# Kernel optimization log

Measured on AMD Instinct MI355X. Metric: run time of the kernel, lower is better.

The kernel has to match this reference:

```python
import jax, jax.numpy as jnp
import numpy as np

B, Q, N, K, C = 32, 500, 200, 16, 92
CLASS_COST, POLY_COST, GIOU_COST = 1.0, 5.0, 1.0
EPS = 1e-6


def setup_inputs() -> dict:
    key = jax.random.key(0)
    k1, k2, k3, k4 = jax.random.split(key, 4)
    return {
        "pred_logits": jax.random.normal(k1, (B, Q, C), dtype=jnp.float32),
        "pred_polylines": jax.random.uniform(k2, (B, Q, K, 2), dtype=jnp.float32),
        "tgt_labels": jax.random.randint(k3, (B, N), 0, 91, dtype=jnp.int32),
        "tgt_polylines": jax.random.uniform(k4, (B, N, K, 2), dtype=jnp.float32),
    }


def _poly_to_bbox(p):
    # p: (..., K, 2) -> (..., 4) xyxy
    x, y = p[..., 0], p[..., 1]
    return jnp.stack([x.min(-1), y.min(-1), x.max(-1), y.max(-1)], axis=-1)


def _giou(b1, b2):
    # b1: (B,Q,4), b2: (B,N,4) -> (B,Q,N) pairwise generalized IoU
    area1 = jnp.clip(b1[..., 2] - b1[..., 0], 0) * jnp.clip(b1[..., 3] - b1[..., 1], 0)
    area2 = jnp.clip(b2[..., 2] - b2[..., 0], 0) * jnp.clip(b2[..., 3] - b2[..., 1], 0)
    lt = jnp.maximum(b1[:, :, None, :2], b2[:, None, :, :2])
    rb = jnp.minimum(b1[:, :, None, 2:], b2[:, None, :, 2:])
    wh = jnp.clip(rb - lt, 0)
    inter = wh[..., 0] * wh[..., 1]
    union = area1[:, :, None] + area2[:, None, :] - inter
    iou = inter / jnp.maximum(union, EPS)
    lt_c = jnp.minimum(b1[:, :, None, :2], b2[:, None, :, :2])
    rb_c = jnp.maximum(b1[:, :, None, 2:], b2[:, None, :, 2:])
    wh_c = jnp.clip(rb_c - lt_c, 0)
    area_c = wh_c[..., 0] * wh_c[..., 1]
    return iou - (area_c - union) / jnp.maximum(area_c, EPS)


def reference(pred_logits, pred_polylines, tgt_labels, tgt_polylines):
    # Batched matching cost matrix C: (B, Q, N). The host-side scipy Hungarian
    # solve in the original consumes this matrix; the GPU math being kerneled
    # is exactly this cost computation.
    b, q, k = pred_polylines.shape[0], pred_polylines.shape[1], pred_polylines.shape[2]
    n = tgt_labels.shape[1]
    two_k = 2 * k

    prob = jax.nn.softmax(pred_logits, axis=-1)  # (B,Q,C)
    idx = jnp.broadcast_to(tgt_labels[:, None, :], (b, q, n))
    cost_class = -jnp.take_along_axis(prob, idx, axis=2)  # (B,Q,N)

    out_flat = pred_polylines.reshape(b, q, two_k)
    tgt_flat = tgt_polylines.reshape(b, n, two_k)
    tgt_rev = jnp.flip(tgt_polylines, axis=2).reshape(b, n, two_k)
    # L1 cdist, normalized by 2K; take min over polyline orientation
    cost_fwd = jnp.abs(out_flat[:, :, None, :] - tgt_flat[:, None, :, :]).sum(-1) / float(two_k)
    cost_rev = jnp.abs(out_flat[:, :, None, :] - tgt_rev[:, None, :, :]).sum(-1) / float(two_k)
    cost_poly = jnp.minimum(cost_fwd, cost_rev)

    out_bbox = _poly_to_bbox(pred_polylines)  # (B,Q,4)
    tgt_bbox = _poly_to_bbox(tgt_polylines)   # (B,N,4)
    cost_giou = -_giou(out_bbox, tgt_bbox)    # (B,Q,N)

    return CLASS_COST * cost_class + POLY_COST * cost_poly + GIOU_COST * cost_giou
```

## Files before the change

### kernel.cpp

```cpp
#include <hip/hip_runtime.h>
#include <math.h>

constexpr int B_ = 32, Q_ = 500, N_ = 200, K_ = 16, C_ = 92;
constexpr int TWO_K = 2 * K_;
constexpr int WAVES = 8;
constexpr int THREADS = 64 * WAVES;
constexpr int TPAD = 34;
constexpr float EPS_ = 1e-6f;
constexpr float POLY_SCALE = 5.0f / 32.0f;

__device__ __forceinline__ float rfl(float v) {
    return __int_as_float(__builtin_amdgcn_readfirstlane(__float_as_int(v)));
}

__global__ __launch_bounds__(THREADS, 8)
void matcher_cost_kernel(const float* __restrict__ logits,
                         const float* __restrict__ ppoly,
                         const int*   __restrict__ labels,
                         const float* __restrict__ tpoly,
                         float* __restrict__ out)
{
    __shared__ float sT[N_ * TPAD];
    __shared__ float sTB[N_ * 5];
    __shared__ int   sLbl[N_];
    __shared__ float sProb[WAVES * C_];

    const int tid  = threadIdx.x;
    const int b    = blockIdx.y;
    const int q0   = blockIdx.x * WAVES;
    const int w    = tid >> 6;
    const int lane = tid & 63;
    const int q    = q0 + w;

    {
        const float* tb_base = tpoly + (size_t)b * (N_ * TWO_K);
        for (int u = tid; u < N_ * TWO_K / 4; u += THREADS) {
            float4 v = reinterpret_cast<const float4*>(tb_base)[u];
            int n = u >> 3;
            int j = (u & 7) * 4;
            float* d = &sT[n * TPAD + j];
            reinterpret_cast<float2*>(d)[0] = make_float2(v.x, v.y);
            reinterpret_cast<float2*>(d)[1] = make_float2(v.z, v.w);
        }
        for (int n = tid; n < N_; n += THREADS) sLbl[n] = labels[b * N_ + n];
    }
    __syncthreads();

    for (int n = tid; n < N_; n += THREADS) {
        const float2* tr = reinterpret_cast<const float2*>(&sT[n * TPAD]);
        float xm = INFINITY, ym = INFINITY, xM = -INFINITY, yM = -INFINITY;
        #pragma unroll
        for (int k = 0; k < K_; ++k) {
            float2 t = tr[k];
            xm = fminf(xm, t.x); xM = fmaxf(xM, t.x);
            ym = fminf(ym, t.y); yM = fmaxf(yM, t.y);
        }
        sTB[n * 5 + 0] = xm; sTB[n * 5 + 1] = ym;
        sTB[n * 5 + 2] = xM; sTB[n * 5 + 3] = yM;
        sTB[n * 5 + 4] = (xM - xm) * (yM - ym);
    }
    __syncthreads();

    if (q >= Q_) return;

    const int wq = __builtin_amdgcn_readfirstlane(q);
    const float* pp = ppoly + ((size_t)(b * Q_ + wq)) * TWO_K;
    float pfs[TWO_K];
    #pragma unroll
    for (int j = 0; j < TWO_K; ++j) pfs[j] = rfl(pp[j]);

    float pxm, pym, pxM, pyM;
    {
        float2 p = reinterpret_cast<const float2*>(pp)[lane & 15];
        float xm = p.x, xM = p.x, ym = p.y, yM = p.y;
        #pragma unroll
        for (int off = 8; off; off >>= 1) {
            xm = fminf(xm, __shfl_xor(xm, off));
            xM = fmaxf(xM, __shfl_xor(xM, off));
            ym = fminf(ym, __shfl_xor(ym, off));
            yM = fmaxf(yM, __shfl_xor(yM, off));
        }
        pxm = rfl(xm); pxM = rfl(xM); pym = rfl(ym); pyM = rfl(yM);
    }
    const float parea = (pxM - pxm) * (pyM - pym);

    {
        const float* lg = logits + ((size_t)(b * Q_ + wq)) * C_;
        float lv0 = lg[lane];
        float lv1 = (lane < C_ - 64) ? lg[64 + lane] : -INFINITY;
        float m = fmaxf(lv0, lv1);
        #pragma unroll
        for (int off = 32; off; off >>= 1) m = fmaxf(m, __shfl_xor(m, off));
        float e0 = __expf(lv0 - m);
        float e1 = (lane < C_ - 64) ? __expf(lv1 - m) : 0.0f;
        float s = e0 + e1;
        #pragma unroll
        for (int off = 32; off; off >>= 1) s += __shfl_xor(s, off);
        float rs = 1.0f / s;
        sProb[w * C_ + lane] = e0 * rs;
        if (lane < C_ - 64) sProb[w * C_ + 64 + lane] = e1 * rs;
    }

    float* outRow = out + ((size_t)(b * Q_ + wq)) * N_;
    const float* probRow = &sProb[w * C_];

    for (int i = 0; i < (N_ + 63) / 64; ++i) {
        int n = lane + 64 * i;
        if (n >= N_) break;
        const float2* tr = reinterpret_cast<const float2*>(&sT[n * TPAD]);
        float f0 = 0.0f, f1 = 0.0f, r0 = 0.0f, r1 = 0.0f;
        #pragma unroll
        for (int k = 0; k < K_; ++k) {
            float2 t = tr[k];
            float a = fabsf(pfs[2 * k]     - t.x) + fabsf(pfs[2 * k + 1] - t.y);
            float c = fabsf(pfs[30 - 2 * k] - t.x) + fabsf(pfs[31 - 2 * k] - t.y);
            if (k & 1) { f1 += a; r1 += c; } else { f0 += a; r0 += c; }
        }
        float cpoly = fminf(f0 + f1, r0 + r1) * POLY_SCALE;

        float cclass = -probRow[sLbl[n]];

        float tx0 = sTB[n * 5 + 0], ty0 = sTB[n * 5 + 1];
        float tx1 = sTB[n * 5 + 2], ty1 = sTB[n * 5 + 3];
        float tarea = sTB[n * 5 + 4];
        float ix0 = fmaxf(pxm, tx0), iy0 = fmaxf(pym, ty0);
        float ix1 = fminf(pxM, tx1), iy1 = fminf(pyM, ty1);
        float iw = fmaxf(ix1 - ix0, 0.0f), ih = fmaxf(iy1 - iy0, 0.0f);
        float inter = iw * ih;
        float uni = parea + tarea - inter;
        float iou = inter / fmaxf(uni, EPS_);
        float cx0 = fminf(pxm, tx0), cy0 = fminf(pym, ty0);
        float cx1 = fmaxf(pxM, tx1), cy1 = fmaxf(pyM, ty1);
        float ca = (cx1 - cx0) * (cy1 - cy0);
        float giou = iou - (ca - uni) / fmaxf(ca, EPS_);

        outRow[n] = cclass + cpoly - giou;
    }
}

extern "C" void kernel_launch(void* const* d_in, const int* in_sizes, int n_in,
                              void* d_out, int out_size, void* d_ws, size_t ws_size,
                              hipStream_t stream) {
    const float* logits = (const float*)d_in[0];
    const float* ppoly  = (const float*)d_in[1];
    const int*   labels = (const int*)d_in[2];
    const float* tpoly  = (const float*)d_in[3];
    float* out = (float*)d_out;

    dim3 grid((Q_ + WAVES - 1) / WAVES, B_);
    matcher_cost_kernel<<<grid, THREADS, 0, stream>>>(logits, ppoly, labels, tpoly, out);
}
```

Measured before the change: 29.27 us.

## Retile matcher kernel into query-by-target blocks with lanes over queries

```diff
diff --git a/kernel.cpp b/kernel.cpp
--- a/kernel.cpp
+++ b/kernel.cpp
@@ -3,126 +3,129 @@
 
 constexpr int B_ = 32, Q_ = 500, N_ = 200, K_ = 16, C_ = 92;
 constexpr int TWO_K = 2 * K_;
+constexpr int QT = 64;
+constexpr int NG = 50;
 constexpr int WAVES = 8;
 constexpr int THREADS = 64 * WAVES;
-constexpr int TPAD = 34;
+constexpr int PS = 93;
+constexpr int OS = 51;
 constexpr float EPS_ = 1e-6f;
 constexpr float POLY_SCALE = 5.0f / 32.0f;
 
-__device__ __forceinline__ float rfl(float v) {
-    return __int_as_float(__builtin_amdgcn_readfirstlane(__float_as_int(v)));
-}
-
-__global__ __launch_bounds__(THREADS, 8)
+__global__ __launch_bounds__(THREADS)
 void matcher_cost_kernel(const float* __restrict__ logits,
                          const float* __restrict__ ppoly,
                          const int*   __restrict__ labels,
                          const float* __restrict__ tpoly,
                          float* __restrict__ out)
 {
-    __shared__ float sT[N_ * TPAD];
-    __shared__ float sTB[N_ * 5];
-    __shared__ int   sLbl[N_];
-    __shared__ float sProb[WAVES * C_];
+    __shared__ float sProb[QT * PS];
+    __shared__ float sOut[QT * OS];
+    __shared__ float sTB[NG * 5];
 
     const int tid  = threadIdx.x;
-    const int b    = blockIdx.y;
-    const int q0   = blockIdx.x * WAVES;
     const int w    = tid >> 6;
     const int lane = tid & 63;
-    const int q    = q0 + w;
+    const int qt   = blockIdx.x;
+    const int ng   = blockIdx.y;
+    const int b    = blockIdx.z;
+    const int q0   = qt * QT;
+    const int n0   = ng * NG;
 
     {
-        const float* tb_base = tpoly + (size_t)b * (N_ * TWO_K);
-        for (int u = tid; u < N_ * TWO_K / 4; u += THREADS) {
-            float4 v = reinterpret_cast<const float4*>(tb_base)[u];
-            int n = u >> 3;
-            int j = (u & 7) * 4;
-            float* d = &sT[n * TPAD + j];
-            reinterpret_cast<float2*>(d)[0] = make_float2(v.x, v.y);
-            reinterpret_cast<float2*>(d)[1] = make_float2(v.z, v.w);
+        int g = tid >> 3, sub = tid & 7;
+        int qq = q0 + g; if (qq >= Q_) qq = Q_ - 1;
+        const float* lg = logits + ((size_t)(b * Q_ + qq)) * C_;
+        float v[12]; float mx = -INFINITY;
+        #pragma unroll
+        for (int m = 0; m < 12; ++m) {
+            int c = sub + 8 * m;
+            if (c < C_) { v[m] = lg[c]; mx = fmaxf(mx, v[m]); } else v[m] = -INFINITY;
         }
-        for (int n = tid; n < N_; n += THREADS) sLbl[n] = labels[b * N_ + n];
+        #pragma unroll
+        for (int off = 4; off; off >>= 1) mx = fmaxf(mx, __shfl_xor(mx, off, 8));
+        float s = 0.0f;
+        #pragma unroll
+        for (int m = 0; m < 12; ++m) {
+            int c = sub + 8 * m;
+            if (c < C_) { v[m] = __expf(v[m] - mx); s += v[m]; }
+        }
+        #pragma unroll
+        for (int off = 4; off; off >>= 1) s += __shfl_xor(s, off, 8);
+        float rs = 1.0f / s;
+        #pragma unroll
+        for (int m = 0; m < 12; ++m) {
+            int c = sub + 8 * m;
+            if (c < C_) sProb[g * PS + c] = v[m] * rs;
+        }
     }
+
+    {
+        int g = tid >> 3, sub = tid & 7;
+        if (g < NG) {
+            const float4* tr = reinterpret_cast<const float4*>(
+                tpoly + ((size_t)(b * N_ + n0 + g)) * TWO_K);
+            float4 p = tr[sub];
+            float xm = fminf(p.x, p.z), xM = fmaxf(p.x, p.z);
+            float ym = fminf(p.y, p.w), yM = fmaxf(p.y, p.w);
+            #pragma unroll
+            for (int off = 4; off; off >>= 1) {
+                xm = fminf(xm, __shfl_xor(xm, off, 8));
+                xM = fmaxf(xM, __shfl_xor(xM, off, 8));
+                ym = fminf(ym, __shfl_xor(ym, off, 8));
+                yM = fmaxf(yM, __shfl_xor(yM, off, 8));
+            }
+            if (sub == 0) {
+                sTB[g * 5 + 0] = xm; sTB[g * 5 + 1] = ym;
+                sTB[g * 5 + 2] = xM; sTB[g * 5 + 3] = yM;
+                sTB[g * 5 + 4] = (xM - xm) * (yM - ym);
+            }
+        }
+    }
+
+    int qc = q0 + lane; if (qc >= Q_) qc = Q_ - 1;
+    float px[K_], py[K_];
+    float pxm = INFINITY, pxM = -INFINITY, pym = INFINITY, pyM = -INFINITY;
+    {
+        const float4* pr = reinterpret_cast<const float4*>(
+            ppoly + ((size_t)(b * Q_ + qc)) * TWO_K);
+        #pragma unroll
+        for (int j = 0; j < 8; ++j) {
+            float4 v = pr[j];
+            px[2 * j] = v.x;  py[2 * j] = v.y;
+            px[2 * j + 1] = v.z; py[2 * j + 1] = v.w;
+            pxm = fminf(pxm, fminf(v.x, v.z)); pxM = fmaxf(pxM, fmaxf(v.x, v.z));
+            pym = fminf(pym, fminf(v.y, v.w)); pyM = fmaxf(pyM, fmaxf(v.y, v.w));
+        }
+    }
+    const float parea = (pxM - pxm) * (pyM - pym);
     __syncthreads();
 
-    for (int n = tid; n < N_; n += THREADS) {
-        const float2* tr = reinterpret_cast<const float2*>(&sT[n * TPAD]);
-        float xm = INFINITY, ym = INFINITY, xM = -INFINITY, yM = -INFINITY;
+    const int probbase = lane * PS;
+
+    for (int nn = w; nn < NG; nn += WAVES) {
+        const int nu = __builtin_amdgcn_readfirstlane(n0 + nn);
+        const float* __restrict__ tr = tpoly + ((size_t)(b * N_ + nu)) * TWO_K;
+        float ts[TWO_K];
+        #pragma unroll
+        for (int j = 0; j < TWO_K; ++j) ts[j] = tr[j];
+        const int lbl = labels[b * N_ + nu];
+
+        float f0 = 0, f1 = 0, r0 = 0, r1 = 0;
         #pragma unroll
         for (int k = 0; k < K_; ++k) {
-            float2 t = tr[k];
-            xm = fminf(xm, t.x); xM = fmaxf(xM, t.x);
-            ym = fminf(ym, t.y); yM = fmaxf(yM, t.y);
+            float tx = ts[2 * k], ty = ts[2 * k + 1];
+            float af = fabsf(px[k] - tx) + fabsf(py[k] - ty);
+            float ar = fabsf(px[K_ - 1 - k] - tx) + fabsf(py[K_ - 1 - k] - ty);
+            if (k & 1) { f1 += af; r1 += ar; } else { f0 += af; r0 += ar; }
         }
-        sTB[n * 5 + 0] = xm; sTB[n * 5 + 1] = ym;
-        sTB[n * 5 + 2] = xM; sTB[n * 5 + 3] = yM;
-        sTB[n * 5 + 4] = (xM - xm) * (yM - ym);
-    }
-    __syncthreads();
+        float cpoly = fminf(f0 + f1, r0 + r1);
 
-    if (q >= Q_) return;
+        float cclass = -sProb[probbase + lbl];
 
-    const int wq = __builtin_amdgcn_readfirstlane(q);
-    const float* pp = ppoly + ((size_t)(b * Q_ + wq)) * TWO_K;
-    float pfs[TWO_K];
-    #pragma unroll
-    for (int j = 0; j < TWO_K; ++j) pfs[j] = rfl(pp[j]);
-
-    float pxm, pym, pxM, pyM;
-    {
-        float2 p = reinterpret_cast<const float2*>(pp)[lane & 15];
-        float xm = p.x, xM = p.x, ym = p.y, yM = p.y;
-        #pragma unroll
-        for (int off = 8; off; off >>= 1) {
-            xm = fminf(xm, __shfl_xor(xm, off));
-            xM = fmaxf(xM, __shfl_xor(xM, off));
-            ym = fminf(ym, __shfl_xor(ym, off));
-            yM = fmaxf(yM, __shfl_xor(yM, off));
-        }
-        pxm = rfl(xm); pxM = rfl(xM); pym = rfl(ym); pyM = rfl(yM);
-    }
-    const float parea = (pxM - pxm) * (pyM - pym);
-
-    {
-        const float* lg = logits + ((size_t)(b * Q_ + wq)) * C_;
-        float lv0 = lg[lane];
-        float lv1 = (lane < C_ - 64) ? lg[64 + lane] : -INFINITY;
-        float m = fmaxf(lv0, lv1);
-        #pragma unroll
-        for (int off = 32; off; off >>= 1) m = fmaxf(m, __shfl_xor(m, off));
-        float e0 = __expf(lv0 - m);
-        float e1 = (lane < C_ - 64) ? __expf(lv1 - m) : 0.0f;
-        float s = e0 + e1;
-        #pragma unroll
-        for (int off = 32; off; off >>= 1) s += __shfl_xor(s, off);
-        float rs = 1.0f / s;
-        sProb[w * C_ + lane] = e0 * rs;
-        if (lane < C_ - 64) sProb[w * C_ + 64 + lane] = e1 * rs;
-    }
-
-    float* outRow = out + ((size_t)(b * Q_ + wq)) * N_;
-    const float* probRow = &sProb[w * C_];
-
-    for (int i = 0; i < (N_ + 63) / 64; ++i) {
-        int n = lane + 64 * i;
-        if (n >= N_) break;
-        const float2* tr = reinterpret_cast<const float2*>(&sT[n * TPAD]);
-        float f0 = 0.0f, f1 = 0.0f, r0 = 0.0f, r1 = 0.0f;
-        #pragma unroll
-        for (int k = 0; k < K_; ++k) {
-            float2 t = tr[k];
-            float a = fabsf(pfs[2 * k]     - t.x) + fabsf(pfs[2 * k + 1] - t.y);
-            float c = fabsf(pfs[30 - 2 * k] - t.x) + fabsf(pfs[31 - 2 * k] - t.y);
-            if (k & 1) { f1 += a; r1 += c; } else { f0 += a; r0 += c; }
-        }
-        float cpoly = fminf(f0 + f1, r0 + r1) * POLY_SCALE;
-
-        float cclass = -probRow[sLbl[n]];
-
-        float tx0 = sTB[n * 5 + 0], ty0 = sTB[n * 5 + 1];
-        float tx1 = sTB[n * 5 + 2], ty1 = sTB[n * 5 + 3];
-        float tarea = sTB[n * 5 + 4];
+        float tx0 = sTB[nn * 5 + 0], ty0 = sTB[nn * 5 + 1];
+        float tx1 = sTB[nn * 5 + 2], ty1 = sTB[nn * 5 + 3];
+        float tarea = sTB[nn * 5 + 4];
         float ix0 = fmaxf(pxm, tx0), iy0 = fmaxf(pym, ty0);
         float ix1 = fminf(pxM, tx1), iy1 = fminf(pyM, ty1);
         float iw = fmaxf(ix1 - ix0, 0.0f), ih = fmaxf(iy1 - iy0, 0.0f);
@@ -134,7 +137,14 @@
         float ca = (cx1 - cx0) * (cy1 - cy0);
         float giou = iou - (ca - uni) / fmaxf(ca, EPS_);
 
-        outRow[n] = cclass + cpoly - giou;
+        sOut[lane * OS + nn] = fmaf(cpoly, POLY_SCALE, cclass) - giou;
+    }
+    __syncthreads();
+
+    for (int r = w; r < QT; r += WAVES) {
+        int q = q0 + r;
+        if (q < Q_ && lane < NG)
+            out[((size_t)(b * Q_ + q)) * N_ + n0 + lane] = sOut[r * OS + lane];
     }
 }
 
@@ -147,6 +157,6 @@
     const float* tpoly  = (const float*)d_in[3];
     float* out = (float*)d_out;
 
-    dim3 grid((Q_ + WAVES - 1) / WAVES, B_);
+    dim3 grid((Q_ + QT - 1) / QT, N_ / NG, B_);
     matcher_cost_kernel<<<grid, THREADS, 0, stream>>>(logits, ppoly, labels, tpoly, out);
 }
```

Measured after the change: 36.57 us. 24.9% more time.

## Process two queries per wave and stage predictions and softmax in shared memory

Applied to the files above, without the earlier changes.

```diff
diff --git a/kernel.cpp b/kernel.cpp
--- a/kernel.cpp
+++ b/kernel.cpp
@@ -3,17 +3,23 @@
 
 constexpr int B_ = 32, Q_ = 500, N_ = 200, K_ = 16, C_ = 92;
 constexpr int TWO_K = 2 * K_;
+constexpr int QT = 16;
 constexpr int WAVES = 8;
 constexpr int THREADS = 64 * WAVES;
 constexpr int TPAD = 34;
+constexpr int PS = 93;
 constexpr float EPS_ = 1e-6f;
 constexpr float POLY_SCALE = 5.0f / 32.0f;
 
 __device__ __forceinline__ float rfl(float v) {
     return __int_as_float(__builtin_amdgcn_readfirstlane(__float_as_int(v)));
 }
-
-__global__ __launch_bounds__(THREADS, 8)
+__device__ __forceinline__ float rcpf_(float x) { return __builtin_amdgcn_rcpf(x); }
+__device__ __forceinline__ float ad(float2 p, float2 t) {
+    return fabsf(p.x - t.x) + fabsf(p.y - t.y);
+}
+
+__global__ __launch_bounds__(THREADS, 4)
 void matcher_cost_kernel(const float* __restrict__ logits,
                          const float* __restrict__ ppoly,
                          const int*   __restrict__ labels,
@@ -21,28 +27,64 @@
                          float* __restrict__ out)
 {
     __shared__ float sT[N_ * TPAD];
+    __shared__ float sP[QT * TPAD];
     __shared__ float sTB[N_ * 5];
+    __shared__ float sPB[QT * 5];
+    __shared__ float sProb[QT * PS];
     __shared__ int   sLbl[N_];
-    __shared__ float sProb[WAVES * C_];
 
     const int tid  = threadIdx.x;
-    const int b    = blockIdx.y;
-    const int q0   = blockIdx.x * WAVES;
     const int w    = tid >> 6;
     const int lane = tid & 63;
-    const int q    = q0 + w;
+    const int b    = blockIdx.y;
+    const int q0   = blockIdx.x * QT;
 
     {
-        const float* tb_base = tpoly + (size_t)b * (N_ * TWO_K);
+        const float* tb = tpoly + (size_t)b * (N_ * TWO_K);
         for (int u = tid; u < N_ * TWO_K / 4; u += THREADS) {
-            float4 v = reinterpret_cast<const float4*>(tb_base)[u];
-            int n = u >> 3;
-            int j = (u & 7) * 4;
+            float4 v = reinterpret_cast<const float4*>(tb)[u];
+            int n = u >> 3, j = (u & 7) * 4;
             float* d = &sT[n * TPAD + j];
             reinterpret_cast<float2*>(d)[0] = make_float2(v.x, v.y);
             reinterpret_cast<float2*>(d)[1] = make_float2(v.z, v.w);
         }
+        if (tid < QT * TWO_K / 4) {
+            int ql = tid >> 3, j = (tid & 7) * 4;
+            int q = min(q0 + ql, Q_ - 1);
+            float4 v = reinterpret_cast<const float4*>(
+                ppoly + (size_t)(b * Q_ + q) * TWO_K)[tid & 7];
+            float* d = &sP[ql * TPAD + j];
+            reinterpret_cast<float2*>(d)[0] = make_float2(v.x, v.y);
+            reinterpret_cast<float2*>(d)[1] = make_float2(v.z, v.w);
+        }
         for (int n = tid; n < N_; n += THREADS) sLbl[n] = labels[b * N_ + n];
+
+        int qi = tid >> 5, l32 = tid & 31;
+        int q = min(q0 + qi, Q_ - 1);
+        const float* lg = logits + (size_t)(b * Q_ + q) * C_;
+        float lv[3]; float m = -INFINITY;
+        #pragma unroll
+        for (int j = 0; j < 3; ++j) {
+            int c = l32 + 32 * j;
+            lv[j] = (c < C_) ? lg[c] : -INFINITY;
+            m = fmaxf(m, lv[j]);
+        }
+        #pragma unroll
+        for (int off = 16; off; off >>= 1) m = fmaxf(m, __shfl_xor(m, off, 32));
+        float s = 0.0f;
+        #pragma unroll
+        for (int j = 0; j < 3; ++j) {
+            int c = l32 + 32 * j;
+            if (c < C_) { float e = __expf(lv[j] - m); lv[j] = e; s += e; }
+        }
+        #pragma unroll
+        for (int off = 16; off; off >>= 1) s += __shfl_xor(s, off, 32);
+        float rs = 1.0f / s;
+        #pragma unroll
+        for (int j = 0; j < 3; ++j) {
+            int c = l32 + 32 * j;
+            if (c < C_) sProb[qi * PS + c] = lv[j] * rs;
+        }
     }
     __syncthreads();
 
@@ -59,82 +101,96 @@
         sTB[n * 5 + 2] = xM; sTB[n * 5 + 3] = yM;
         sTB[n * 5 + 4] = (xM - xm) * (yM - ym);
     }
+    if (tid >= 256 && tid < 256 + QT) {
+        int ql = tid - 256;
+        const float2* pr = reinterpret_cast<const float2*>(&sP[ql * TPAD]);
+        float xm = INFINITY, ym = INFINITY, xM = -INFINITY, yM = -INFINITY;
+        #pragma unroll
+        for (int k = 0; k < K_; ++k) {
+            float2 p = pr[k];
+            xm = fminf(xm, p.x); xM = fmaxf(xM, p.x);
+            ym = fminf(ym, p.y); yM = fmaxf(yM, p.y);
+        }
+        sPB[ql * 5 + 0] = xm; sPB[ql * 5 + 1] = ym;
+        sPB[ql * 5 + 2] = xM; sPB[ql * 5 + 3] = yM;
+        sPB[ql * 5 + 4] = (xM - xm) * (yM - ym);
+    }
     __syncthreads();
 
-    if (q >= Q_) return;
-
-    const int wq = __builtin_amdgcn_readfirstlane(q);
-    const float* pp = ppoly + ((size_t)(b * Q_ + wq)) * TWO_K;
-    float pfs[TWO_K];
-    #pragma unroll
-    for (int j = 0; j < TWO_K; ++j) pfs[j] = rfl(pp[j]);
-
-    float pxm, pym, pxM, pyM;
-    {
-        float2 p = reinterpret_cast<const float2*>(pp)[lane & 15];
-        float xm = p.x, xM = p.x, ym = p.y, yM = p.y;
-        #pragma unroll
-        for (int off = 8; off; off >>= 1) {
-            xm = fminf(xm, __shfl_xor(xm, off));
-            xM = fmaxf(xM, __shfl_xor(xM, off));
-            ym = fminf(ym, __shfl_xor(ym, off));
-            yM = fmaxf(yM, __shfl_xor(yM, off));
-        }
-        pxm = rfl(xm); pxM = rfl(xM); pym = rfl(ym); pyM = rfl(yM);
-    }
-    const float parea = (pxM - pxm) * (pyM - pym);
-
-    {
-        const float* lg = logits + ((size_t)(b * Q_ + wq)) * C_;
-        float lv0 = lg[lane];
-        float lv1 = (lane < C_ - 64) ? lg[64 + lane] : -INFINITY;
-        float m = fmaxf(lv0, lv1);
-        #pragma unroll
-        for (int off = 32; off; off >>= 1) m = fmaxf(m, __shfl_xor(m, off));
-        float e0 = __expf(lv0 - m);
-        float e1 = (lane < C_ - 64) ? __expf(lv1 - m) : 0.0f;
-        float s = e0 + e1;
-        #pragma unroll
-        for (int off = 32; off; off >>= 1) s += __shfl_xor(s, off);
-        float rs = 1.0f / s;
-        sProb[w * C_ + lane] = e0 * rs;
-        if (lane < C_ - 64) sProb[w * C_ + 64 + lane] = e1 * rs;
-    }
-
-    float* outRow = out + ((size_t)(b * Q_ + wq)) * N_;
-    const float* probRow = &sProb[w * C_];
-
-    for (int i = 0; i < (N_ + 63) / 64; ++i) {
-        int n = lane + 64 * i;
-        if (n >= N_) break;
-        const float2* tr = reinterpret_cast<const float2*>(&sT[n * TPAD]);
-        float f0 = 0.0f, f1 = 0.0f, r0 = 0.0f, r1 = 0.0f;
-        #pragma unroll
-        for (int k = 0; k < K_; ++k) {
-            float2 t = tr[k];
-            float a = fabsf(pfs[2 * k]     - t.x) + fabsf(pfs[2 * k + 1] - t.y);
-            float c = fabsf(pfs[30 - 2 * k] - t.x) + fabsf(pfs[31 - 2 * k] - t.y);
-            if (k & 1) { f1 += a; r1 += c; } else { f0 += a; r0 += c; }
-        }
-        float cpoly = fminf(f0 + f1, r0 + r1) * POLY_SCALE;
-
-        float cclass = -probRow[sLbl[n]];
-
-        float tx0 = sTB[n * 5 + 0], ty0 = sTB[n * 5 + 1];
-        float tx1 = sTB[n * 5 + 2], ty1 = sTB[n * 5 + 3];
-        float tarea = sTB[n * 5 + 4];
-        float ix0 = fmaxf(pxm, tx0), iy0 = fmaxf(pym, ty0);
-        float ix1 = fminf(pxM, tx1), iy1 = fminf(pyM, ty1);
+    const int qlA = 2 * w, qlB = 2 * w + 1;
+    const int qA = q0 + qlA, qB = q0 + qlB;
+    if (qA >= Q_) return;
+    const bool vB = (qB < Q_);
+
+    const float Axm = rfl(sPB[qlA * 5 + 0]), Aym = rfl(sPB[qlA * 5 + 1]);
+    const float AxM = rfl(sPB[qlA * 5 + 2]), AyM = rfl(sPB[qlA * 5 + 3]);
+    const float Aar = rfl(sPB[qlA * 5 + 4]);
+    const float Bxm = rfl(sPB[qlB * 5 + 0]), Bym = rfl(sPB[qlB * 5 + 1]);
+    const float BxM = rfl(sPB[qlB * 5 + 2]), ByM = rfl(sPB[qlB * 5 + 3]);
+    const float Bar = rfl(sPB[qlB * 5 + 4]);
+
+    const float2* pa = reinterpret_cast<const float2*>(&sP[qlA * TPAD]);
+    const float2* pb = reinterpret_cast<const float2*>(&sP[qlB * TPAD]);
+    float* outA = out + (size_t)(b * Q_ + qA) * N_;
+    float* outB = out + (size_t)(b * Q_ + min(qB, Q_ - 1)) * N_;
+
+    for (int i = 0; i < 4; ++i) {
+        int n_ = 64 * i + lane;
+        int nn = min(n_, N_ - 1);
+        const float2* tr = reinterpret_cast<const float2*>(&sT[nn * TPAD]);
+
+        float fA0 = 0, fA1 = 0, rA0 = 0, rA1 = 0;
+        float fB0 = 0, fB1 = 0, rB0 = 0, rB1 = 0;
+        #pragma unroll
+        for (int k = 0; k < 8; ++k) {
+            const int k2 = 15 - k;
+            float2 t1 = tr[k],  t2 = tr[k2];
+            float2 a1 = pa[k],  a2 = pa[k2];
+            float2 b1 = pb[k],  b2 = pb[k2];
+            fA0 += ad(a1, t1);  fA1 += ad(a2, t2);
+            rA0 += ad(a2, t1);  rA1 += ad(a1, t2);
+            fB0 += ad(b1, t1);  fB1 += ad(b2, t2);
+            rB0 += ad(b2, t1);  rB1 += ad(b1, t2);
+        }
+        float cpA = fminf(fA0 + fA1, rA0 + rA1);
+        float cpB = fminf(fB0 + fB1, rB0 + rB1);
+
+        int lbl = sLbl[nn];
+        float prA = sProb[qlA * PS + lbl];
+        float prB = sProb[qlB * PS + lbl];
+
+        float tx0 = sTB[nn * 5 + 0], ty0 = sTB[nn * 5 + 1];
+        float tx1 = sTB[nn * 5 + 2], ty1 = sTB[nn * 5 + 3];
+        float ta  = sTB[nn * 5 + 4];
+
+        float ix0 = fmaxf(Axm, tx0), iy0 = fmaxf(Aym, ty0);
+        float ix1 = fminf(AxM, tx1), iy1 = fminf(AyM, ty1);
         float iw = fmaxf(ix1 - ix0, 0.0f), ih = fmaxf(iy1 - iy0, 0.0f);
         float inter = iw * ih;
-        float uni = parea + tarea - inter;
-        float iou = inter / fmaxf(uni, EPS_);
-        float cx0 = fminf(pxm, tx0), cy0 = fminf(pym, ty0);
-        float cx1 = fmaxf(pxM, tx1), cy1 = fmaxf(pyM, ty1);
+        float uni = Aar + ta - inter;
+        float iou = inter * rcpf_(fmaxf(uni, EPS_));
+        float cx0 = fminf(Axm, tx0), cy0 = fminf(Aym, ty0);
+        float cx1 = fmaxf(AxM, tx1), cy1 = fmaxf(AyM, ty1);
         float ca = (cx1 - cx0) * (cy1 - cy0);
-        float giou = iou - (ca - uni) / fmaxf(ca, EPS_);
-
-        outRow[n] = cclass + cpoly - giou;
+        float giouA = iou - (ca - uni) * rcpf_(fmaxf(ca, EPS_));
+
+        float jx0 = fmaxf(Bxm, tx0), jy0 = fmaxf(Bym, ty0);
+        float jx1 = fminf(BxM, tx1), jy1 = fminf(ByM, ty1);
+        float jw = fmaxf(jx1 - jx0, 0.0f), jh = fmaxf(jy1 - jy0, 0.0f);
+        float interB = jw * jh;
+        float uniB = Bar + ta - interB;
+        float iouB = interB * rcpf_(fmaxf(uniB, EPS_));
+        float dx0 = fminf(Bxm, tx0), dy0 = fminf(Bym, ty0);
+        float dx1 = fmaxf(BxM, tx1), dy1 = fmaxf(ByM, ty1);
+        float cb = (dx1 - dx0) * (dy1 - dy0);
+        float giouB = iouB - (cb - uniB) * rcpf_(fmaxf(cb, EPS_));
+
+        float oA = fmaf(cpA, POLY_SCALE, -prA) - giouA;
+        float oB = fmaf(cpB, POLY_SCALE, -prB) - giouB;
+        if (n_ < N_) {
+            outA[n_] = oA;
+            if (vB) outB[n_] = oB;
+        }
     }
 }
 
@@ -147,6 +203,6 @@
     const float* tpoly  = (const float*)d_in[3];
     float* out = (float*)d_out;
 
-    dim3 grid((Q_ + WAVES - 1) / WAVES, B_);
+    dim3 grid((Q_ + QT - 1) / QT, B_);
     matcher_cost_kernel<<<grid, THREADS, 0, stream>>>(logits, ppoly, labels, tpoly, out);
 }
```

After: 34.05 us. +16.4%, slower.
